# Kernel tuning notes

Hardware: AMD Instinct MI355X
Metric: run time of the kernel (lower is better)

Reference implementation:

```python
import jax, jax.numpy as jnp
import numpy as np

K = 1.0            # curvature (manifold.k); sqrt(K)=1 simplifies formulas
EPS = 1e-5         # module eps used in variance rescale
MIN_NORM = 1e-8    # clamp for sqrt of Lorentz inners
MAX_EUCLID = 10.0  # rescale_to_max_euclid cap (keeps cosh/sinh in fp32 range)


def l_inner(x, y):
    # Lorentz inner product <x,y>_L = -x0*y0 + <x_s, y_s>, keepdim
    return -x[..., :1] * y[..., :1] + jnp.sum(x[..., 1:] * y[..., 1:], axis=-1, keepdims=True)


def centroid(x):
    # Lorentzian centroid over the group axis (dim=-2)
    avg = jnp.mean(x, axis=-2, keepdims=True)
    denom = jnp.sqrt(jnp.clip(-l_inner(avg, avg), MIN_NORM, None))
    return avg / denom


def logmap(x, y):
    alpha = jnp.clip(-l_inner(x, y), 1.0 + 1e-7, None)   # -<x,y>_L >= 1
    dist = jnp.arccosh(alpha)
    nomin = y - alpha * x                                # y + <x,y>_L * x
    denom = jnp.sqrt(jnp.clip(l_inner(nomin, nomin), MIN_NORM, None))
    return dist * nomin / denom


def _plus_origin(p):
    # p + o where o = (1, 0, ..., 0)
    return jnp.concatenate([p[..., :1] + 1.0, p[..., 1:]], axis=-1)


def transp0back(x, v):
    # parallel transport of tangent v at x back to the origin o
    nom = -v[..., :1]                 # <o, v>_L = -v0
    denom = 1.0 + x[..., :1]          # K - <x, o>_L = 1 + x0
    return v + (nom / denom) * _plus_origin(x)


def transp0(y, v):
    # parallel transport of tangent v at origin o to point y
    nom = l_inner(y, v)
    denom = 1.0 + y[..., :1]          # K - <o, y>_L = 1 + y0
    return v + (nom / denom) * _plus_origin(y)


def rescale_to_max_euclid(u):
    n = jnp.linalg.norm(u, axis=-1, keepdims=True)
    scale = jnp.minimum(1.0, MAX_EUCLID / jnp.clip(n, MIN_NORM, None))
    return u * scale


def expmap(x, u):
    nrm = jnp.sqrt(jnp.clip(l_inner(u, u), MIN_NORM, None))
    return jnp.cosh(nrm) * x + jnp.sinh(nrm) * (u / nrm)


def setup_inputs() -> dict:
    key = jax.random.key(0)
    k1, = jax.random.split(key, 1)
    bs, h, w, c = 64, 56, 56, 128
    # sample spatial components, lift onto the hyperboloid: x0 = sqrt(1+|xs|^2)
    xs = 0.5 * jax.random.normal(k1, (bs, h, w, c - 1), dtype=jnp.float32)
    x0 = jnp.sqrt(1.0 + jnp.sum(xs * xs, axis=-1, keepdims=True))
    x = jnp.concatenate([x0, xs], axis=-1)
    gamma = jnp.ones((c,), dtype=jnp.float32)
    # beta = manifold.origin(c) = (1, 0, ..., 0)
    beta = jnp.zeros((c,), dtype=jnp.float32).at[0].set(1.0)
    return {"x": x, "gamma": gamma, "beta": beta, "groups": 8}


def reference(x, gamma, beta, groups):
    bs, h, w, c = x.shape
    xg = x.reshape(bs, -1, groups, c)                    # (bs, hw/g, g, c)
    mean = centroid(xg)                                  # (bs, hw/g, 1, c)
    x_T = logmap(mean, xg)                               # tangent at mean
    x_T = transp0back(mean, x_T)                         # tangent at origin
    # Frechet-style variance: mean Euclidean norm over spatial dim (dim=1)
    var = jnp.mean(jnp.linalg.norm(x_T, axis=-1, keepdims=True), axis=1, keepdims=True)
    x_T = x_T * (gamma / (var + EPS))
    x_T = rescale_to_max_euclid(x_T)
    x_T = transp0(beta, x_T)                             # transport to beta
    out = expmap(beta, x_T)
    return out.reshape(bs, h, w, c)
```

## Files before the change

kernel.cpp:

```cpp
#include <hip/hip_runtime.h>
#include <math.h>


constexpr int S_GROUPS = 392;
constexpr int NSL = 16;
constexpr int N_GROUPS = 64 * S_GROUPS;

__device__ __forceinline__ float rsum8(float v) {
  v += __shfl_xor(v, 1, 64);
  v += __shfl_xor(v, 2, 64);
  v += __shfl_xor(v, 4, 64);
  return v;
}

__device__ __forceinline__ void lorentz_xt(const float* __restrict__ gp,
                                           int lane, float* __restrict__ smrow,
                                           float v[16], float xt[16]) {
  const int p = lane >> 3, q = lane & 7;
  const float* base = gp + p * 128 + q * 16;
#pragma unroll
  for (int j = 0; j < 4; ++j)
    *reinterpret_cast<float4*>(&v[4 * j]) =
        *reinterpret_cast<const float4*>(base + 4 * j);

  float a8[8];
  {
    const bool hi = (lane & 32) != 0;
#pragma unroll
    for (int i = 0; i < 8; ++i) {
      float kp = hi ? v[i + 8] : v[i];
      float sd = hi ? v[i] : v[i + 8];
      a8[i] = kp + __shfl_xor(sd, 32, 64);
    }
  }
  float a4[4];
  {
    const bool hi = (lane & 16) != 0;
#pragma unroll
    for (int i = 0; i < 4; ++i) {
      float kp = hi ? a8[i + 4] : a8[i];
      float sd = hi ? a8[i] : a8[i + 4];
      a4[i] = kp + __shfl_xor(sd, 16, 64);
    }
  }
  float c0, c1;
  {
    const bool hi = (lane & 8) != 0;
    float kp0 = hi ? a4[2] : a4[0], sd0 = hi ? a4[0] : a4[2];
    float kp1 = hi ? a4[3] : a4[1], sd1 = hi ? a4[1] : a4[3];
    c0 = kp0 + __shfl_xor(sd0, 8, 64);
    c1 = kp1 + __shfl_xor(sd1, 8, 64);
  }
  *reinterpret_cast<float2*>(&smrow[q * 16 + p * 2]) =
      make_float2(c0 * 0.125f, c1 * 0.125f);
  __syncthreads();
  float mean[16];
#pragma unroll
  for (int j = 0; j < 4; ++j)
    *reinterpret_cast<float4*>(&mean[4 * j]) =
        *reinterpret_cast<const float4*>(&smrow[q * 16 + 4 * j]);

  float part = 0.f;
#pragma unroll
  for (int i = 0; i < 16; ++i) part += mean[i] * mean[i];
  if (q == 0) part -= 2.f * mean[0] * mean[0];
  float ia = rsum8(part);
  float rden = rsqrtf(fmaxf(-ia, 1e-8f));
#pragma unroll
  for (int i = 0; i < 16; ++i) mean[i] *= rden;
  float mean0 = __shfl(mean[0], 0, 64);
  float y0p = __shfl(v[0], lane & 56, 64);

  float dp = 0.f;
#pragma unroll
  for (int i = 0; i < 16; ++i) dp += mean[i] * v[i];
  if (q == 0) dp -= 2.f * mean[0] * v[0];
  dp = rsum8(dp);
  float alpha = fmaxf(-dp, 1.f + 1e-7f);
  float t = alpha - 1.f;
  float dist = log1pf(t + sqrtf(t * (alpha + 1.f)));

  float nm[16];
  float ip = 0.f;
#pragma unroll
  for (int i = 0; i < 16; ++i) {
    nm[i] = v[i] - alpha * mean[i];
    ip += nm[i] * nm[i];
  }
  if (q == 0) ip -= 2.f * nm[0] * nm[0];
  float inn = rsum8(ip);
  float sc = dist * rsqrtf(fmaxf(inn, 1e-8f));

  float xt0 = sc * (y0p - alpha * mean0);
  float coef = -xt0 / (1.f + mean0);
#pragma unroll
  for (int i = 0; i < 16; ++i) xt[i] = sc * nm[i] + coef * mean[i];
  if (q == 0) xt[0] += coef;
}

__global__ __launch_bounds__(256) void lngn_pass1(const float* __restrict__ x,
                                                  float* __restrict__ var_acc) {
  __shared__ float sm[4][128];
  const int w = threadIdx.x >> 6;
  const int lane = threadIdx.x & 63;
  const int wid = blockIdx.x * 4 + w;
  float v[16], xt[16];
  lorentz_xt(x + (size_t)wid * 1024, lane, sm[w], v, xt);
  float ns = 0.f;
#pragma unroll
  for (int i = 0; i < 16; ++i) ns += xt[i] * xt[i];
  ns = rsum8(ns);
  const int p = lane >> 3, q = lane & 7;
  if (q == 0) {
    int b = wid / S_GROUPS;
    atomicAdd(&var_acc[(b * 8 + p) * NSL + (wid & (NSL - 1))], sqrtf(ns));
  }
}

__global__ __launch_bounds__(256) void lngn_finalize(
    const float* __restrict__ var_acc, float* __restrict__ var_out) {
  int i = blockIdx.x * 256 + threadIdx.x;
  float s = 0.f;
#pragma unroll
  for (int j = 0; j < NSL; ++j) s += var_acc[i * NSL + j];
  var_out[i] = s * (1.f / (float)S_GROUPS);
}

__global__ __launch_bounds__(256) void lngn_pass2(
    const float* __restrict__ x, const float* __restrict__ gamma,
    const float* __restrict__ beta, const float* __restrict__ var,
    float* __restrict__ out) {
  __shared__ float sm[4][128];
  const int w = threadIdx.x >> 6;
  const int lane = threadIdx.x & 63;
  const int wid = blockIdx.x * 4 + w;
  const int p = lane >> 3, q = lane & 7;
  float v[16], xt[16];
  lorentz_xt(x + (size_t)wid * 1024, lane, sm[w], v, xt);

  const int b = wid / S_GROUPS;
  float s1 = 1.f / (var[b * 8 + p] + 1e-5f);

  float gm[16];
#pragma unroll
  for (int j = 0; j < 4; ++j)
    *reinterpret_cast<float4*>(&gm[4 * j]) =
        *reinterpret_cast<const float4*>(gamma + q * 16 + 4 * j);
  float u[16];
  float nsq = 0.f;
#pragma unroll
  for (int i = 0; i < 16; ++i) {
    u[i] = xt[i] * gm[i] * s1;
    nsq += u[i] * u[i];
  }
  nsq = rsum8(nsq);
  float n = sqrtf(nsq);
  float scl = fminf(1.f, 10.f / fmaxf(n, 1e-8f));

  float bt[16];
#pragma unroll
  for (int j = 0; j < 4; ++j)
    *reinterpret_cast<float4*>(&bt[4 * j]) =
        *reinterpret_cast<const float4*>(beta + q * 16 + 4 * j);
  float beta0 = __shfl(bt[0], 0, 64);

  float np = 0.f;
#pragma unroll
  for (int i = 0; i < 16; ++i) {
    u[i] *= scl;
    np += bt[i] * u[i];
  }
  if (q == 0) np -= 2.f * bt[0] * u[0];
  float nom = rsum8(np);
  float c2 = nom / (1.f + beta0);
  float ip = 0.f;
#pragma unroll
  for (int i = 0; i < 16; ++i) {
    u[i] += c2 * bt[i];
    ip += u[i] * u[i];
  }
  if (q == 0) {
    u[0] += c2;
    ip -= 2.f * (u[0] - c2) * (u[0] - c2);
    ip += u[0] * u[0] - (u[0] - c2) * (u[0] - c2);
    ip -= 2.f * u[0] * u[0] + 2.f * (u[0] - c2) * (u[0] - c2) -
          2.f * (u[0] - c2) * (u[0] - c2);
  }
  ip = 0.f;
#pragma unroll
  for (int i = 0; i < 16; ++i) ip += u[i] * u[i];
  if (q == 0) ip -= 2.f * u[0] * u[0];
  float inn = rsum8(ip);

  float nrm = sqrtf(fmaxf(inn, 1e-8f));
  float e = expf(nrm), ie = 1.f / e;
  float chv = 0.5f * (e + ie);
  float isn = (0.5f * (e - ie)) / nrm;
  float o[16];
#pragma unroll
  for (int i = 0; i < 16; ++i) o[i] = chv * bt[i] + isn * u[i];
  float* ob = out + (size_t)wid * 1024 + p * 128 + q * 16;
#pragma unroll
  for (int j = 0; j < 4; ++j)
    *reinterpret_cast<float4*>(ob + 4 * j) =
        *reinterpret_cast<const float4*>(&o[4 * j]);
}

extern "C" void kernel_launch(void* const* d_in, const int* in_sizes, int n_in,
                              void* d_out, int out_size, void* d_ws,
                              size_t ws_size, hipStream_t stream) {
  const float* x = (const float*)d_in[0];
  const float* gamma = (const float*)d_in[1];
  const float* beta = (const float*)d_in[2];
  float* out = (float*)d_out;
  float* var_acc = (float*)d_ws;
  float* var_final = var_acc + 512 * NSL;

  hipMemsetAsync(var_acc, 0, 512 * NSL * sizeof(float), stream);
  lngn_pass1<<<N_GROUPS / 4, 256, 0, stream>>>(x, var_acc);
  lngn_finalize<<<2, 256, 0, stream>>>(var_acc, var_final);
  lngn_pass2<<<N_GROUPS / 4, 256, 0, stream>>>(x, gamma, beta, var_final, out);
}
```

Baseline: 229.3 us.

## Algebraically fuse Lorentz reductions, drop atomics and block barriers

The per-group math is rewritten so the three dot products (mean-mean, mean-x, x-x) come out of a single fused three-way shuffle reduction, and the logmap, transport and norm terms are rebuilt from those scalars instead of from extra per-element passes and reductions. Pass 1 now has each wave handle two groups and writes per-group norms to a partial buffer rather than using atomics. That removes the memset, and a wave-parallel finalize reduces the buffer. Block-wide __syncthreads is replaced by a wave-level barrier, since each wave only touches its own LDS row. Pass 2 likewise folds the rescale, transport and expmap inner products into closed-form scalars, at the risk of extra floating-point cancellation in those expanded formulas.

```diff
diff --git a/kernel.cpp b/kernel.cpp
--- a/kernel.cpp
+++ b/kernel.cpp
@@ -3,127 +3,144 @@
 
 
 constexpr int S_GROUPS = 392;
-constexpr int NSL = 16;
 constexpr int N_GROUPS = 64 * S_GROUPS;
 
-__device__ __forceinline__ float rsum8(float v) {
-  v += __shfl_xor(v, 1, 64);
-  v += __shfl_xor(v, 2, 64);
-  v += __shfl_xor(v, 4, 64);
-  return v;
-}
-
-__device__ __forceinline__ void lorentz_xt(const float* __restrict__ gp,
-                                           int lane, float* __restrict__ smrow,
-                                           float v[16], float xt[16]) {
+__device__ __forceinline__ void wave_lds_fence() {
+  __asm__ volatile("" ::: "memory");
+  __builtin_amdgcn_wave_barrier();
+  __asm__ volatile("" ::: "memory");
+}
+
+__device__ __forceinline__ void rsum8x3(float& a, float& b, float& c) {
+#pragma unroll
+  for (int m = 1; m <= 4; m <<= 1) {
+    a += __shfl_xor(a, m, 64);
+    b += __shfl_xor(b, m, 64);
+    c += __shfl_xor(c, m, 64);
+  }
+}
+
+__device__ __forceinline__ void fold_mean(const float v[16], int lane,
+                                          float& c0, float& c1) {
+  float a8[8];
+  const bool h5 = (lane & 32) != 0;
+#pragma unroll
+  for (int i = 0; i < 8; ++i) {
+    float kp = h5 ? v[i + 8] : v[i];
+    float sd = h5 ? v[i] : v[i + 8];
+    a8[i] = kp + __shfl_xor(sd, 32, 64);
+  }
+  float a4[4];
+  const bool h4 = (lane & 16) != 0;
+#pragma unroll
+  for (int i = 0; i < 4; ++i) {
+    float kp = h4 ? a8[i + 4] : a8[i];
+    float sd = h4 ? a8[i] : a8[i + 4];
+    a4[i] = kp + __shfl_xor(sd, 16, 64);
+  }
+  const bool h3 = (lane & 8) != 0;
+  float kp0 = h3 ? a4[2] : a4[0], sd0 = h3 ? a4[0] : a4[2];
+  float kp1 = h3 ? a4[3] : a4[1], sd1 = h3 ? a4[1] : a4[3];
+  c0 = (kp0 + __shfl_xor(sd0, 8, 64)) * 0.125f;
+  c1 = (kp1 + __shfl_xor(sd1, 8, 64)) * 0.125f;
+}
+
+struct CoreOut {
+  float avg[16];
+  float sc, k, coef;
+  float iaL, dpL, yyE, y0p, avg0;
+};
+
+__device__ __forceinline__ void core(const float v[16], int lane,
+                                     float* __restrict__ smrow, CoreOut& o) {
   const int p = lane >> 3, q = lane & 7;
-  const float* base = gp + p * 128 + q * 16;
+  float c0, c1;
+  fold_mean(v, lane, c0, c1);
+  *reinterpret_cast<float2*>(&smrow[q * 16 + p * 2]) = make_float2(c0, c1);
+  wave_lds_fence();
 #pragma unroll
   for (int j = 0; j < 4; ++j)
-    *reinterpret_cast<float4*>(&v[4 * j]) =
-        *reinterpret_cast<const float4*>(base + 4 * j);
-
-  float a8[8];
-  {
-    const bool hi = (lane & 32) != 0;
-#pragma unroll
-    for (int i = 0; i < 8; ++i) {
-      float kp = hi ? v[i + 8] : v[i];
-      float sd = hi ? v[i] : v[i + 8];
-      a8[i] = kp + __shfl_xor(sd, 32, 64);
-    }
-  }
-  float a4[4];
-  {
-    const bool hi = (lane & 16) != 0;
-#pragma unroll
-    for (int i = 0; i < 4; ++i) {
-      float kp = hi ? a8[i + 4] : a8[i];
-      float sd = hi ? a8[i] : a8[i + 4];
-      a4[i] = kp + __shfl_xor(sd, 16, 64);
-    }
-  }
-  float c0, c1;
-  {
-    const bool hi = (lane & 8) != 0;
-    float kp0 = hi ? a4[2] : a4[0], sd0 = hi ? a4[0] : a4[2];
-    float kp1 = hi ? a4[3] : a4[1], sd1 = hi ? a4[1] : a4[3];
-    c0 = kp0 + __shfl_xor(sd0, 8, 64);
-    c1 = kp1 + __shfl_xor(sd1, 8, 64);
-  }
-  *reinterpret_cast<float2*>(&smrow[q * 16 + p * 2]) =
-      make_float2(c0 * 0.125f, c1 * 0.125f);
-  __syncthreads();
-  float mean[16];
-#pragma unroll
-  for (int j = 0; j < 4; ++j)
-    *reinterpret_cast<float4*>(&mean[4 * j]) =
+    *reinterpret_cast<float4*>(&o.avg[4 * j]) =
         *reinterpret_cast<const float4*>(&smrow[q * 16 + 4 * j]);
-
-  float part = 0.f;
-#pragma unroll
-  for (int i = 0; i < 16; ++i) part += mean[i] * mean[i];
-  if (q == 0) part -= 2.f * mean[0] * mean[0];
-  float ia = rsum8(part);
-  float rden = rsqrtf(fmaxf(-ia, 1e-8f));
-#pragma unroll
-  for (int i = 0; i < 16; ++i) mean[i] *= rden;
-  float mean0 = __shfl(mean[0], 0, 64);
-  float y0p = __shfl(v[0], lane & 56, 64);
-
-  float dp = 0.f;
-#pragma unroll
-  for (int i = 0; i < 16; ++i) dp += mean[i] * v[i];
-  if (q == 0) dp -= 2.f * mean[0] * v[0];
-  dp = rsum8(dp);
-  float alpha = fmaxf(-dp, 1.f + 1e-7f);
+  wave_lds_fence();
+
+  float pa = 0.f, pd = 0.f, py = 0.f;
+#pragma unroll
+  for (int i = 0; i < 16; ++i) {
+    pa = fmaf(o.avg[i], o.avg[i], pa);
+    pd = fmaf(o.avg[i], v[i], pd);
+    py = fmaf(v[i], v[i], py);
+  }
+  if (q == 0) {
+    pa -= 2.f * o.avg[0] * o.avg[0];
+    pd -= 2.f * o.avg[0] * v[0];
+  }
+  rsum8x3(pa, pd, py);
+  o.iaL = pa;
+  o.dpL = pd;
+  o.yyE = py;
+  o.y0p = __shfl(v[0], lane & 56, 64);
+  o.avg0 = __shfl(o.avg[0], 0, 64);
+
+  float rden = rsqrtf(fmaxf(-pa, 1e-8f));
+  float a_raw = -pd * rden;
+  float alpha = fmaxf(a_raw, 1.f + 1e-7f);
   float t = alpha - 1.f;
   float dist = log1pf(t + sqrtf(t * (alpha + 1.f)));
-
-  float nm[16];
-  float ip = 0.f;
-#pragma unroll
-  for (int i = 0; i < 16; ++i) {
-    nm[i] = v[i] - alpha * mean[i];
-    ip += nm[i] * nm[i];
-  }
-  if (q == 0) ip -= 2.f * nm[0] * nm[0];
-  float inn = rsum8(ip);
-  float sc = dist * rsqrtf(fmaxf(inn, 1e-8f));
-
-  float xt0 = sc * (y0p - alpha * mean0);
-  float coef = -xt0 / (1.f + mean0);
-#pragma unroll
-  for (int i = 0; i < 16; ++i) xt[i] = sc * nm[i] + coef * mean[i];
-  if (q == 0) xt[0] += coef;
+  float yyL = py - 2.f * o.y0p * o.y0p;
+  float inn = fmaxf(yyL + 2.f * alpha * a_raw - alpha * alpha, 1e-8f);
+  o.sc = dist * rsqrtf(inn);
+  float am = alpha * rden;
+  float mean0 = rden * o.avg0;
+  float v0 = o.sc * (o.y0p - am * o.avg0);
+  o.coef = -v0 / (1.f + mean0);
+  o.k = o.coef * rden - o.sc * am;
+}
+
+__device__ __forceinline__ float xt_norm(const CoreOut& A) {
+  float yavgE = A.dpL + 2.f * A.avg0 * A.y0p;
+  float aaE = A.iaL + 2.f * A.avg0 * A.avg0;
+  float nsq = A.sc * A.sc * A.yyE + A.k * A.k * aaE + 2.f * A.sc * A.k * yavgE +
+              A.coef * A.coef + 2.f * A.coef * (A.sc * A.y0p + A.k * A.avg0);
+  return sqrtf(fmaxf(nsq, 0.f));
 }
 
 __global__ __launch_bounds__(256) void lngn_pass1(const float* __restrict__ x,
-                                                  float* __restrict__ var_acc) {
-  __shared__ float sm[4][128];
-  const int w = threadIdx.x >> 6;
+                                                  float* __restrict__ var_part) {
+  __shared__ float sm[4][2][128];
+  const int w = threadIdx.x >> 6, lane = threadIdx.x & 63;
+  const int p = lane >> 3, q = lane & 7;
+  const int wid0 = (blockIdx.x * 4 + w) * 2;
+  const float* b0 = x + (size_t)wid0 * 1024 + p * 128 + q * 16;
+  float vA[16], vB[16];
+#pragma unroll
+  for (int j = 0; j < 4; ++j) {
+    *reinterpret_cast<float4*>(&vA[4 * j]) =
+        *reinterpret_cast<const float4*>(b0 + 4 * j);
+    *reinterpret_cast<float4*>(&vB[4 * j]) =
+        *reinterpret_cast<const float4*>(b0 + 1024 + 4 * j);
+  }
+  CoreOut A, B;
+  core(vA, lane, sm[w][0], A);
+  core(vB, lane, sm[w][1], B);
+  float nA = xt_norm(A), nB = xt_norm(B);
+  if (q == 0) {
+    var_part[(size_t)wid0 * 8 + p] = nA;
+    var_part[(size_t)(wid0 + 1) * 8 + p] = nB;
+  }
+}
+
+__global__ __launch_bounds__(256) void lngn_finalize(
+    const float* __restrict__ var_part, float* __restrict__ var_out) {
+  const int wv = (int)((blockIdx.x * 256 + threadIdx.x) >> 6);
   const int lane = threadIdx.x & 63;
-  const int wid = blockIdx.x * 4 + w;
-  float v[16], xt[16];
-  lorentz_xt(x + (size_t)wid * 1024, lane, sm[w], v, xt);
-  float ns = 0.f;
-#pragma unroll
-  for (int i = 0; i < 16; ++i) ns += xt[i] * xt[i];
-  ns = rsum8(ns);
-  const int p = lane >> 3, q = lane & 7;
-  if (q == 0) {
-    int b = wid / S_GROUPS;
-    atomicAdd(&var_acc[(b * 8 + p) * NSL + (wid & (NSL - 1))], sqrtf(ns));
-  }
-}
-
-__global__ __launch_bounds__(256) void lngn_finalize(
-    const float* __restrict__ var_acc, float* __restrict__ var_out) {
-  int i = blockIdx.x * 256 + threadIdx.x;
+  const int b = wv >> 3, p = wv & 7;
+  const float* base = var_part + (size_t)b * S_GROUPS * 8 + p;
   float s = 0.f;
-#pragma unroll
-  for (int j = 0; j < NSL; ++j) s += var_acc[i * NSL + j];
-  var_out[i] = s * (1.f / (float)S_GROUPS);
+  for (int s0 = lane; s0 < S_GROUPS; s0 += 64) s += base[(size_t)s0 * 8];
+#pragma unroll
+  for (int m = 32; m >= 1; m >>= 1) s += __shfl_xor(s, m, 64);
+  if (lane == 0) var_out[wv] = s * (1.f / (float)S_GROUPS);
 }
 
 __global__ __launch_bounds__(256) void lngn_pass2(
@@ -131,79 +148,68 @@
     const float* __restrict__ beta, const float* __restrict__ var,
     float* __restrict__ out) {
   __shared__ float sm[4][128];
-  const int w = threadIdx.x >> 6;
-  const int lane = threadIdx.x & 63;
+  const int w = threadIdx.x >> 6, lane = threadIdx.x & 63;
+  const int p = lane >> 3, q = lane & 7;
   const int wid = blockIdx.x * 4 + w;
-  const int p = lane >> 3, q = lane & 7;
-  float v[16], xt[16];
-  lorentz_xt(x + (size_t)wid * 1024, lane, sm[w], v, xt);
+  const size_t base = (size_t)wid * 1024 + p * 128 + q * 16;
+  float v[16];
+#pragma unroll
+  for (int j = 0; j < 4; ++j)
+    *reinterpret_cast<float4*>(&v[4 * j]) =
+        *reinterpret_cast<const float4*>(x + base + 4 * j);
+  CoreOut C;
+  core(v, lane, sm[w], C);
 
   const int b = wid / S_GROUPS;
-  float s1 = 1.f / (var[b * 8 + p] + 1e-5f);
-
-  float gm[16];
-#pragma unroll
-  for (int j = 0; j < 4; ++j)
+  const float s1 = 1.f / (var[b * 8 + p] + 1e-5f);
+  float gm[16], bt[16];
+#pragma unroll
+  for (int j = 0; j < 4; ++j) {
     *reinterpret_cast<float4*>(&gm[4 * j]) =
         *reinterpret_cast<const float4*>(gamma + q * 16 + 4 * j);
-  float u[16];
-  float nsq = 0.f;
-#pragma unroll
-  for (int i = 0; i < 16; ++i) {
-    u[i] = xt[i] * gm[i] * s1;
-    nsq += u[i] * u[i];
-  }
-  nsq = rsum8(nsq);
-  float n = sqrtf(nsq);
-  float scl = fminf(1.f, 10.f / fmaxf(n, 1e-8f));
-
-  float bt[16];
-#pragma unroll
-  for (int j = 0; j < 4; ++j)
     *reinterpret_cast<float4*>(&bt[4 * j]) =
         *reinterpret_cast<const float4*>(beta + q * 16 + 4 * j);
-  float beta0 = __shfl(bt[0], 0, 64);
-
-  float np = 0.f;
+  }
+
+  float u[16];
+  float pe = 0.f, pb = 0.f, pbb = 0.f;
 #pragma unroll
   for (int i = 0; i < 16; ++i) {
-    u[i] *= scl;
-    np += bt[i] * u[i];
-  }
-  if (q == 0) np -= 2.f * bt[0] * u[0];
-  float nom = rsum8(np);
-  float c2 = nom / (1.f + beta0);
-  float ip = 0.f;
-#pragma unroll
-  for (int i = 0; i < 16; ++i) {
-    u[i] += c2 * bt[i];
-    ip += u[i] * u[i];
+    float xt = fmaf(C.sc, v[i], C.k * C.avg[i]);
+    if (i == 0) xt += (q == 0) ? C.coef : 0.f;
+    u[i] = xt * (gm[i] * s1);
+    pe = fmaf(u[i], u[i], pe);
+    pb = fmaf(bt[i], u[i], pb);
+    pbb = fmaf(bt[i], bt[i], pbb);
   }
   if (q == 0) {
-    u[0] += c2;
-    ip -= 2.f * (u[0] - c2) * (u[0] - c2);
-    ip += u[0] * u[0] - (u[0] - c2) * (u[0] - c2);
-    ip -= 2.f * u[0] * u[0] + 2.f * (u[0] - c2) * (u[0] - c2) -
-          2.f * (u[0] - c2) * (u[0] - c2);
-  }
-  ip = 0.f;
-#pragma unroll
-  for (int i = 0; i < 16; ++i) ip += u[i] * u[i];
-  if (q == 0) ip -= 2.f * u[0] * u[0];
-  float inn = rsum8(ip);
-
-  float nrm = sqrtf(fmaxf(inn, 1e-8f));
+    pb -= 2.f * bt[0] * u[0];
+    pbb -= 2.f * bt[0] * bt[0];
+  }
+  rsum8x3(pe, pb, pbb);
+  const float u0 = __shfl(u[0], 0, 64);
+  const float bt0 = __shfl(bt[0], 0, 64);
+
+  float n = sqrtf(pe);
+  float scl = fminf(1.f, 10.f / fmaxf(n, 1e-8f));
+  float c2 = scl * pb / (1.f + bt0);
+  float uuL = pe - 2.f * u0 * u0;
+  float innw = scl * scl * uuL + 2.f * scl * c2 * (pb - u0) +
+               c2 * c2 * (pbb - 2.f * bt0 - 1.f);
+  float nrm = sqrtf(fmaxf(innw, 1e-8f));
   float e = expf(nrm), ie = 1.f / e;
   float chv = 0.5f * (e + ie);
   float isn = (0.5f * (e - ie)) / nrm;
-  float o[16];
-#pragma unroll
-  for (int i = 0; i < 16; ++i) o[i] = chv * bt[i] + isn * u[i];
-  float* ob = out + (size_t)wid * 1024 + p * 128 + q * 16;
+  float C1 = chv + isn * c2, C2 = isn * scl, C3 = isn * c2;
+  float o16[16];
+#pragma unroll
+  for (int i = 0; i < 16; ++i) o16[i] = fmaf(C1, bt[i], C2 * u[i]);
+  if (q == 0) o16[0] += C3;
+  float* ob = out + base;
 #pragma unroll
   for (int j = 0; j < 4; ++j)
     *reinterpret_cast<float4*>(ob + 4 * j) =
-        *reinterpret_cast<const float4*>(&o[4 * j]);
+        *reinterpret_cast<const float4*>(&o16[4 * j]);
 }
 
 extern "C" void kernel_launch(void* const* d_in, const int* in_sizes, int n_in,
@@ -213,11 +219,10 @@
   const float* gamma = (const float*)d_in[1];
   const float* beta = (const float*)d_in[2];
   float* out = (float*)d_out;
-  float* var_acc = (float*)d_ws;
-  float* var_final = var_acc + 512 * NSL;
-
-  hipMemsetAsync(var_acc, 0, 512 * NSL * sizeof(float), stream);
-  lngn_pass1<<<N_GROUPS / 4, 256, 0, stream>>>(x, var_acc);
-  lngn_finalize<<<2, 256, 0, stream>>>(var_acc, var_final);
+  float* var_part = (float*)d_ws;
+  float* var_final = var_part + (size_t)N_GROUPS * 8;
+
+  lngn_pass1<<<N_GROUPS / 8, 256, 0, stream>>>(x, var_part);
+  lngn_finalize<<<128, 256, 0, stream>>>(var_part, var_final);
   lngn_pass2<<<N_GROUPS / 4, 256, 0, stream>>>(x, gamma, beta, var_final, out);
 }
```

Result: faster. 224.4 us (-2.2%).
